# Kernel tuning notes

Measured on AMD Instinct MI355X. Metric: run time of the kernel, lower is better.

The kernel has to match this reference:

```python
import jax, jax.numpy as jnp
import numpy as np

N = 50000
E = 1600000
F_IN = 256
DIMS = 64
N_CLS = 16
R = 8


def glorot(key, shape):
    fan = shape[-2] + shape[-1] if len(shape) >= 2 else shape[-1] * 2
    std = jnp.sqrt(6.0 / fan)
    return jax.random.uniform(key, shape, jnp.float32, -std, std)


def setup_inputs() -> dict:
    key = jax.random.key(0)
    ks = jax.random.split(key, 12)
    x = jax.random.normal(ks[0], (N, F_IN), jnp.float32)
    edge_index = jax.random.randint(ks[1], (2, E), 0, N)
    edge_weight = jax.random.uniform(ks[2], (E,), jnp.float32)
    edge_color = jax.random.randint(ks[3], (E,), 0, R)
    W1 = glorot(ks[4], (R, F_IN, DIMS))
    atten1 = glorot(ks[5], (R, 2 * DIMS))
    root1 = glorot(ks[6], (F_IN, DIMS))
    bias1 = jnp.zeros((DIMS,), jnp.float32)
    W2 = glorot(ks[7], (R, DIMS, N_CLS))
    atten2 = glorot(ks[8], (R, 2 * N_CLS))
    root2 = glorot(ks[9], (DIMS, N_CLS))
    bias2 = jnp.zeros((N_CLS,), jnp.float32)
    return dict(x=x, edge_index=edge_index, edge_weight=edge_weight,
                edge_color=edge_color, W1=W1, atten1=atten1, root1=root1,
                bias1=bias1, W2=W2, atten2=atten2, root2=root2, bias2=bias2)


def wrgat_conv(x, src, dst, ew, ec, W, atten, root, bias):
    # x: [N, f_in]; W: [R, f_in, d]; atten: [R, 2d]
    d = W.shape[-1]
    xr = jnp.einsum('nf,rfd->rnd', x, W)            # [R, N, d] per-relation projection
    xi = xr[ec, dst]                                 # [E, d] dst (x_i)
    xj = xr[ec, src]                                 # [E, d] src (x_j)
    a_i = atten[:, :d][ec]                           # [E, d]
    a_j = atten[:, d:][ec]
    s = jnp.sum(a_i * xi + a_j * xj, axis=-1)        # [E]
    s = jax.nn.leaky_relu(s, 0.2)
    # segment softmax over (relation, destination) groups
    seg = ec * N + dst                               # [E], each edge belongs to one relation
    nseg = R * N
    m = jax.ops.segment_max(s, seg, num_segments=nseg)
    m = jnp.where(jnp.isfinite(m), m, 0.0)           # empty segments -> 0
    e = jnp.exp(s - m[seg])
    denom = jax.ops.segment_sum(e, seg, num_segments=nseg)
    alpha = e / jnp.maximum(denom[seg], 1e-16)
    msg = (alpha * ew)[:, None] * xj                 # [E, d]
    summed = jax.ops.segment_sum(msg, seg, num_segments=nseg).reshape(R, N, d)
    cnt = jax.ops.segment_sum(jnp.ones_like(ew), seg, num_segments=nseg).reshape(R, N, 1)
    out = (summed / jnp.maximum(cnt, 1.0)).sum(axis=0)  # mean aggr per relation, summed over relations
    return out + x @ root + bias


def reference(x, edge_index, edge_weight, edge_color, W1, atten1, root1, bias1,
              W2, atten2, root2, bias2):
    src, dst = edge_index[0], edge_index[1]          # PyG flow source_to_target: x_j=src, x_i=dst
    h = wrgat_conv(x, src, dst, edge_weight, edge_color, W1, atten1, root1, bias1)
    h = jax.nn.relu(h)                               # dropout p=0 -> identity
    h = wrgat_conv(h, src, dst, edge_weight, edge_color, W2, atten2, root2, bias2)
    return jax.nn.log_softmax(h, axis=1)
```

## Files before the change

kernel.cpp:

```cpp
#include <hip/hip_runtime.h>
#include <math.h>

#define N_NODES 50000
#define N_EDGES 1600000
#define F_IN    256
#define DIMS    64
#define N_CLS   16
#define R_REL   8
#define CAP     96

#define PROJ_BLKS 3519
#define CSR_BLKS  6250
#define FRONT_BLKS (PROJ_BLKS + CSR_BLKS)

typedef short bf16x8 __attribute__((ext_vector_type(8)));
typedef float f32x4  __attribute__((ext_vector_type(4)));

__device__ __forceinline__ unsigned short f2bf(float f) {
    unsigned u = __float_as_uint(f);
    unsigned r = (u + 0x7fffu + ((u >> 16) & 1u)) >> 16;
    return (unsigned short)r;
}
__device__ __forceinline__ float bf2f(unsigned short u) {
    return __uint_as_float(((unsigned)u) << 16);
}

__global__ __launch_bounds__(256) void cvt_x_kernel(
        const float* __restrict__ x, ushort* __restrict__ xb) {
    int i4 = blockIdx.x * 256 + threadIdx.x;
    float4 v = ((const float4*)x)[i4];
    ushort4 o;
    o.x = f2bf(v.x); o.y = f2bf(v.y); o.z = f2bf(v.z); o.w = f2bf(v.w);
    ((ushort4*)xb)[i4] = o;
}

__global__ __launch_bounds__(256) void cvt_w_kernel(
        const float* __restrict__ W1, const float* __restrict__ root1,
        ushort* __restrict__ wt1) {
    int idx = blockIdx.x * 256 + threadIdx.x;
    int r = idx >> 14, rem = idx & 16383;
    int n = rem >> 8, k = rem & 255;
    float v = (r < 8) ? W1[((size_t)r * F_IN + k) * DIMS + n]
                      : root1[(size_t)k * DIMS + n];
    wt1[idx] = f2bf(v);
}

#define BM 128
#define XPAD 72
__global__ __launch_bounds__(256, 6) void front_kernel(
        const ushort* __restrict__ xb, const ushort* __restrict__ wt1,
        const float* __restrict__ at1,
        ushort* __restrict__ xr1b, float* __restrict__ hroot,
        float* __restrict__ si1, float* __restrict__ sj1,
        const int* __restrict__ ei, const int* __restrict__ ecol,
        const float* __restrict__ ew, int* __restrict__ fill,
        int2* __restrict__ rec) {
    __shared__ ushort xs[BM][XPAD];
    const int bid = blockIdx.x;
    const int t = threadIdx.x;

    int pb = -1, cb = -1;
    if (bid < 2 * PROJ_BLKS) { if (bid & 1) cb = bid >> 1; else pb = bid >> 1; }
    else cb = PROJ_BLKS + (bid - 2 * PROJ_BLKS);

    if (cb >= 0) {
        int e = cb * 256 + t;
        int s = ei[e], d = ei[N_EDGES + e], c = ecol[e];
        float w_ = ew[e];
        int p = atomicAdd(&fill[d], 1);
        int idx = (p < CAP) ? d * CAP + p : N_NODES * CAP;
        rec[idx] = make_int2(s | (c << 16), __float_as_int(w_));
        return;
    }

    const int r = pb / 391;
    const int node0 = (pb % 391) * BM;
    const ushort* wrow = wt1 + (size_t)r * 64 * 256;

    const int w = t >> 6, lane = t & 63;
    const int lane15 = lane & 15, quad = lane >> 4;

    f32x4 acc[2][4];
    #pragma unroll
    for (int a = 0; a < 2; ++a)
        #pragma unroll
        for (int b = 0; b < 4; ++b)
            acc[a][b] = (f32x4){0.f, 0.f, 0.f, 0.f};

    for (int s = 0; s < 4; ++s) {
        __syncthreads();
        for (int i = t; i < BM * 8; i += 256) {
            int row = i >> 3, k8 = i & 7;
            int node = node0 + row;
            uint4 v = make_uint4(0, 0, 0, 0);
            if (node < N_NODES)
                v = *(const uint4*)&xb[(size_t)node * 256 + s * 64 + k8 * 8];
            *(uint4*)&xs[row][k8 * 8] = v;
        }
        __syncthreads();
        #pragma unroll
        for (int kk = 0; kk < 2; ++kk) {
            int kl = kk * 32 + quad * 8;
            bf16x8 a0 = *(const bf16x8*)&xs[w * 32 + lane15][kl];
            bf16x8 a1 = *(const bf16x8*)&xs[w * 32 + 16 + lane15][kl];
            int kg = s * 64 + kl;
            #pragma unroll
            for (int nt = 0; nt < 4; ++nt) {
                bf16x8 b = *(const bf16x8*)&wrow[(size_t)(nt * 16 + lane15) * 256 + kg];
                acc[0][nt] = __builtin_amdgcn_mfma_f32_16x16x32_bf16(a0, b, acc[0][nt], 0, 0, 0);
                acc[1][nt] = __builtin_amdgcn_mfma_f32_16x16x32_bf16(a1, b, acc[1][nt], 0, 0, 0);
            }
        }
    }

    const float* at = at1 + r * 128;
    #pragma unroll
    for (int mt = 0; mt < 2; ++mt) {
        float pi[4] = {0.f, 0.f, 0.f, 0.f};
        float pj[4] = {0.f, 0.f, 0.f, 0.f};
        #pragma unroll
        for (int nt = 0; nt < 4; ++nt) {
            int gcol = nt * 16 + lane15;
            float ai = 0.f, aj = 0.f;
            if (r < 8) { ai = at[gcol]; aj = at[64 + gcol]; }
            #pragma unroll
            for (int reg = 0; reg < 4; ++reg) {
                float v = acc[mt][nt][reg];
                int grow = node0 + w * 32 + mt * 16 + quad * 4 + reg;
                if (grow < N_NODES) {
                    if (r < 8)
                        xr1b[((size_t)r * N_NODES + grow) * 64 + gcol] = f2bf(v);
                    else
                        hroot[(size_t)grow * 64 + gcol] = v;
                }
                pi[reg] += ai * v;
                pj[reg] += aj * v;
            }
        }
        if (r < 8) {
            #pragma unroll
            for (int reg = 0; reg < 4; ++reg) {
                float s_ = pi[reg], u_ = pj[reg];
                #pragma unroll
                for (int off = 1; off < 16; off <<= 1) {
                    s_ += __shfl_xor(s_, off, 64);
                    u_ += __shfl_xor(u_, off, 64);
                }
                if (lane15 == 0) {
                    int grow = node0 + w * 32 + mt * 16 + quad * 4 + reg;
                    if (grow < N_NODES) {
                        si1[r * N_NODES + grow] = s_;
                        sj1[r * N_NODES + grow] = u_;
                    }
                }
            }
        }
    }
}

__global__ __launch_bounds__(256) void agg1s_kernel(
        const int2* __restrict__ rec, const int* __restrict__ fill,
        const float* __restrict__ si, const float* __restrict__ sj,
        const ushort* __restrict__ xr1b, const float* __restrict__ hroot,
        const float* __restrict__ bias1, float* __restrict__ h) {
    __shared__ int   esrc[4][CAP];
    __shared__ float ecoef[4][CAP];
    __shared__ float sden[4][8];
    __shared__ int   scnt[4][8];
    __shared__ float ssi[4][8];
    const int t = threadIdx.x;
    const int w = t >> 6, lane = t & 63;
    const int d = blockIdx.x * 4 + w;
    if (lane < 8) {
        sden[w][lane] = 0.f; scnt[w][lane] = 0;
        ssi[w][lane] = si[lane * N_NODES + d];
    }
    const int n = min(fill[d], CAP);
    const int base = d * CAP;
    float ex[2] = {0.f, 0.f}, ww[2] = {0.f, 0.f};
    int cc[2] = {0, 0};
    #pragma unroll
    for (int ii = 0; ii < 2; ++ii) {
        int i = lane + ii * 64;
        if (i < n) {
            int2 rc = rec[base + i];
            int s = rc.x & 0xffff, c = rc.x >> 16;
            esrc[w][i] = rc.x;
            float sc = ssi[w][c] + sj[c * N_NODES + s];
            sc = sc > 0.f ? sc : 0.2f * sc;
            float e = __expf(sc);
            ex[ii] = e; cc[ii] = c; ww[ii] = __int_as_float(rc.y);
            atomicAdd(&sden[w][c], e);
            atomicAdd(&scnt[w][c], 1);
        }
    }
    #pragma unroll
    for (int ii = 0; ii < 2; ++ii) {
        int i = lane + ii * 64;
        if (i < n)
            ecoef[w][i] = ex[ii] / fmaxf(sden[w][cc[ii]], 1e-16f)
                          * ww[ii] / (float)scnt[w][cc[ii]];
    }
    float acc0 = 0.f, acc1 = 0.f;
    int i = 0;
    for (; i + 2 <= n; i += 2) {
        int p0 = esrc[w][i], p1 = esrc[w][i + 1];
        float c0 = ecoef[w][i], c1 = ecoef[w][i + 1];
        int r0 = (p0 >> 16) * N_NODES + (p0 & 0xffff);
        int r1 = (p1 >> 16) * N_NODES + (p1 & 0xffff);
        acc0 += c0 * bf2f(xr1b[(size_t)r0 * 64 + lane]);
        acc1 += c1 * bf2f(xr1b[(size_t)r1 * 64 + lane]);
    }
    if (i < n) {
        int p0 = esrc[w][i];
        int r0 = (p0 >> 16) * N_NODES + (p0 & 0xffff);
        acc0 += ecoef[w][i] * bf2f(xr1b[(size_t)r0 * 64 + lane]);
    }
    float acc = acc0 + acc1 + hroot[(size_t)d * 64 + lane] + bias1[lane];
    h[(size_t)d * 64 + lane] = fmaxf(acc, 0.f);
}

__global__ __launch_bounds__(256) void proj2_kernel(
        const float* __restrict__ h, const float* __restrict__ W2,
        const float* __restrict__ atten2, ushort* __restrict__ xr2b,
        float* __restrict__ si2, float* __restrict__ sj2) {
    __shared__ float w2sh[8][64][16];
    __shared__ float a2sh[8][32];
    __shared__ float hsh[32][65];
    const int t = threadIdx.x;
    for (int i = t; i < R_REL * DIMS * N_CLS; i += 256)
        w2sh[i >> 10][(i >> 4) & 63][i & 15] = W2[i];
    if (t < R_REL * 2 * N_CLS) a2sh[t >> 5][t & 31] = atten2[t];
    const int node0 = blockIdx.x * 32;
    for (int i = t; i < 32 * 64; i += 256) {
        int nn = i >> 6, kk = i & 63;
        int node = node0 + nn;
        hsh[nn][kk] = (node < N_NODES) ? h[(size_t)node * 64 + kk] : 0.f;
    }
    __syncthreads();
    const int nl = t & 31, r = t >> 5;
    const int node = node0 + nl;
    float acc[16] = {};
    #pragma unroll 4
    for (int k = 0; k < 64; ++k) {
        float hv = hsh[nl][k];
        #pragma unroll
        for (int c = 0; c < 16; ++c) acc[c] += hv * w2sh[r][k][c];
    }
    if (node < N_NODES) {
        float si = 0.f, sj = 0.f;
        size_t base = ((size_t)r * N_NODES + node) * 16;
        #pragma unroll
        for (int c = 0; c < 16; ++c) {
            si += a2sh[r][c] * acc[c];
            sj += a2sh[r][16 + c] * acc[c];
        }
        #pragma unroll
        for (int c4 = 0; c4 < 4; ++c4) {
            ushort4 o;
            o.x = f2bf(acc[c4 * 4 + 0]); o.y = f2bf(acc[c4 * 4 + 1]);
            o.z = f2bf(acc[c4 * 4 + 2]); o.w = f2bf(acc[c4 * 4 + 3]);
            *(ushort4*)&xr2b[base + c4 * 4] = o;
        }
        si2[r * N_NODES + node] = si;
        sj2[r * N_NODES + node] = sj;
    }
}

__global__ __launch_bounds__(256) void agg2s_kernel(
        const int2* __restrict__ rec, const int* __restrict__ fill,
        const float* __restrict__ si, const float* __restrict__ sj,
        const ushort* __restrict__ xr2b, const float* __restrict__ h,
        const float* __restrict__ root2, const float* __restrict__ bias2,
        float* __restrict__ out) {
    __shared__ float rsh[64][17];
    __shared__ float hsh[4][64];
    __shared__ int   esrc[4][CAP];
    __shared__ float ecoef[4][CAP];
    __shared__ float sden[4][8];
    __shared__ int   scnt[4][8];
    __shared__ float ssi[4][8];
    const int t = threadIdx.x;
    for (int i = t; i < DIMS * N_CLS; i += 256) rsh[i >> 4][i & 15] = root2[i];
    const int w = t >> 6, lane = t & 63;
    const int d = blockIdx.x * 4 + w;
    hsh[w][lane] = h[(size_t)d * 64 + lane];
    if (lane < 8) {
        sden[w][lane] = 0.f; scnt[w][lane] = 0;
        ssi[w][lane] = si[lane * N_NODES + d];
    }
    const int n = min(fill[d], CAP);
    const int base = d * CAP;
    float ex[2] = {0.f, 0.f}, ww[2] = {0.f, 0.f};
    int cc[2] = {0, 0};
    #pragma unroll
    for (int ii = 0; ii < 2; ++ii) {
        int i = lane + ii * 64;
        if (i < n) {
            int2 rc = rec[base + i];
            int s = rc.x & 0xffff, c = rc.x >> 16;
            esrc[w][i] = rc.x;
            float sc = ssi[w][c] + sj[c * N_NODES + s];
            sc = sc > 0.f ? sc : 0.2f * sc;
            float e = __expf(sc);
            ex[ii] = e; cc[ii] = c; ww[ii] = __int_as_float(rc.y);
            atomicAdd(&sden[w][c], e);
            atomicAdd(&scnt[w][c], 1);
        }
    }
    #pragma unroll
    for (int ii = 0; ii < 2; ++ii) {
        int i = lane + ii * 64;
        if (i < n)
            ecoef[w][i] = ex[ii] / fmaxf(sden[w][cc[ii]], 1e-16f)
                          * ww[ii] / (float)scnt[w][cc[ii]];
    }
    __syncthreads();
    const int sub = lane >> 4, cd = lane & 15;
    float acc = 0.f;
    for (int i = sub; i < n; i += 4) {
        int p = esrc[w][i];
        int row = (p >> 16) * N_NODES + (p & 0xffff);
        acc += ecoef[w][i] * bf2f(xr2b[(size_t)row * 16 + cd]);
    }
    #pragma unroll
    for (int k0 = 0; k0 < 16; ++k0) {
        int k = sub * 16 + k0;
        acc += hsh[w][k] * rsh[k][cd];
    }
    acc += __shfl_xor(acc, 16, 64);
    acc += __shfl_xor(acc, 32, 64);
    if (sub == 0) {
        acc += bias2[cd];
        float m = acc;
        #pragma unroll
        for (int off = 8; off; off >>= 1) m = fmaxf(m, __shfl_xor(m, off, 16));
        float ex2 = expf(acc - m);
        float ssum = ex2;
        #pragma unroll
        for (int off = 8; off; off >>= 1) ssum += __shfl_xor(ssum, off, 16);
        out[(size_t)d * 16 + cd] = acc - m - logf(ssum);
    }
}

extern "C" void kernel_launch(void* const* d_in, const int* in_sizes, int n_in,
                              void* d_out, int out_size, void* d_ws, size_t ws_size,
                              hipStream_t stream) {
    const float* x     = (const float*)d_in[0];
    const int*   ei    = (const int*)  d_in[1];
    const float* ew    = (const float*)d_in[2];
    const int*   ecol  = (const int*)  d_in[3];
    const float* W1    = (const float*)d_in[4];
    const float* at1   = (const float*)d_in[5];
    const float* root1 = (const float*)d_in[6];
    const float* b1    = (const float*)d_in[7];
    const float* W2    = (const float*)d_in[8];
    const float* at2   = (const float*)d_in[9];
    const float* root2 = (const float*)d_in[10];
    const float* b2    = (const float*)d_in[11];
    float* out = (float*)d_out;
    float* ws  = (float*)d_ws;

    ushort*   xb    = (ushort*)(ws + 0);
    ushort*   wt1   = (ushort*)(ws + 6400000);
    ushort*   xr1b  = (ushort*)(ws + 6480000);
    float*    hroot = ws + 19280000;
    ushort*   xr2b  = (ushort*)(ws + 22480000);
    float*    si1   = ws + 25680000;
    float*    sj1   = ws + 26080000;
    float*    si2   = ws + 26480000;
    float*    sj2   = ws + 26880000;
    int*      fill  = (int*)(ws + 27280000);
    float*    h     = ws + 27330000;
    int2*     rec   = (int2*)(ws + 30530000);

    hipMemsetAsync(fill, 0, (size_t)N_NODES * 4, stream);

    cvt_x_kernel<<<12500, 256, 0, stream>>>(x, xb);
    cvt_w_kernel<<<576, 256, 0, stream>>>(W1, root1, wt1);
    front_kernel<<<FRONT_BLKS, 256, 0, stream>>>(xb, wt1, at1, xr1b, hroot,
                                                 si1, sj1, ei, ecol, ew, fill, rec);
    agg1s_kernel<<<12500, 256, 0, stream>>>(rec, fill, si1, sj1, xr1b, hroot, b1, h);
    proj2_kernel<<<1563, 256, 0, stream>>>(h, W2, at2, xr2b, si2, sj2);
    agg2s_kernel<<<12500, 256, 0, stream>>>(rec, fill, si2, sj2, xr2b, h, root2, b2, out);
}
```

Baseline: 447.7 us.

## Async global-to-LDS loads with XOR swizzle, nontemporal record stores, deeper gather unroll

The projection GEMM now stages x tiles through global_load_lds async copies into an XOR-swizzled, unpadded LDS layout instead of register round-trips. This removes VGPR staging and keeps LDS reads free of bank conflicts. Out-of-range rows are clamped rather than zero-filled. Edge records are packed into a 64-bit word written with a nontemporal store, and the agg1 gather loop is unrolled to four independent accumulators for more memory-level parallelism.

```diff
diff --git a/kernel.cpp b/kernel.cpp
--- a/kernel.cpp
+++ b/kernel.cpp
@@ -15,6 +15,13 @@
 
 typedef short bf16x8 __attribute__((ext_vector_type(8)));
 typedef float f32x4  __attribute__((ext_vector_type(4)));
+typedef unsigned int u32;
+typedef const __attribute__((address_space(1))) u32* gas_ptr;
+typedef __attribute__((address_space(3))) u32* las_ptr;
+
+__device__ __forceinline__ void async16(const void* g, void* l) {
+    __builtin_amdgcn_global_load_lds((gas_ptr)g, (las_ptr)l, 16, 0, 0);
+}
 
 __device__ __forceinline__ unsigned short f2bf(float f) {
     unsigned u = __float_as_uint(f);
@@ -46,7 +53,6 @@
 }
 
 #define BM 128
-#define XPAD 72
 __global__ __launch_bounds__(256, 6) void front_kernel(
         const ushort* __restrict__ xb, const ushort* __restrict__ wt1,
         const float* __restrict__ at1,
@@ -54,8 +60,8 @@
         float* __restrict__ si1, float* __restrict__ sj1,
         const int* __restrict__ ei, const int* __restrict__ ecol,
         const float* __restrict__ ew, int* __restrict__ fill,
-        int2* __restrict__ rec) {
-    __shared__ ushort xs[BM][XPAD];
+        unsigned long long* __restrict__ rec) {
+    __shared__ ushort xs[BM * 64];
     const int bid = blockIdx.x;
     const int t = threadIdx.x;
 
@@ -69,7 +75,10 @@
         float w_ = ew[e];
         int p = atomicAdd(&fill[d], 1);
         int idx = (p < CAP) ? d * CAP + p : N_NODES * CAP;
-        rec[idx] = make_int2(s | (c << 16), __float_as_int(w_));
+        unsigned long long rv =
+            ((unsigned long long)__float_as_uint(w_) << 32)
+            | (unsigned)(s | (c << 16));
+        __builtin_nontemporal_store(rv, &rec[idx]);
         return;
     }
 
@@ -79,6 +88,8 @@
 
     const int w = t >> 6, lane = t & 63;
     const int lane15 = lane & 15, quad = lane >> 4;
+    const int row0 = w * 32 + lane15;
+    const int sw0 = row0 & 7;
 
     f32x4 acc[2][4];
     #pragma unroll
@@ -89,21 +100,24 @@
 
     for (int s = 0; s < 4; ++s) {
         __syncthreads();
-        for (int i = t; i < BM * 8; i += 256) {
-            int row = i >> 3, k8 = i & 7;
+        #pragma unroll
+        for (int c = 0; c < 4; ++c) {
+            int slot = c * 256 + t;
+            int row = slot >> 3, k8p = slot & 7;
+            int k8 = k8p ^ (row & 7);
             int node = node0 + row;
-            uint4 v = make_uint4(0, 0, 0, 0);
-            if (node < N_NODES)
-                v = *(const uint4*)&xb[(size_t)node * 256 + s * 64 + k8 * 8];
-            *(uint4*)&xs[row][k8 * 8] = v;
+            if (node >= N_NODES) node = N_NODES - 1;
+            async16(&xb[(size_t)node * 256 + s * 64 + k8 * 8],
+                    &xs[(c * 256 + w * 64) * 8]);
         }
         __syncthreads();
         #pragma unroll
         for (int kk = 0; kk < 2; ++kk) {
-            int kl = kk * 32 + quad * 8;
-            bf16x8 a0 = *(const bf16x8*)&xs[w * 32 + lane15][kl];
-            bf16x8 a1 = *(const bf16x8*)&xs[w * 32 + 16 + lane15][kl];
-            int kg = s * 64 + kl;
+            int k8 = kk * 4 + quad;
+            int aidx = row0 * 64 + ((k8 ^ sw0) << 3);
+            bf16x8 a0 = *(const bf16x8*)&xs[aidx];
+            bf16x8 a1 = *(const bf16x8*)&xs[aidx + 16 * 64];
+            int kg = s * 64 + kk * 32 + quad * 8;
             #pragma unroll
             for (int nt = 0; nt < 4; ++nt) {
                 bf16x8 b = *(const bf16x8*)&wrow[(size_t)(nt * 16 + lane15) * 256 + kg];
@@ -159,7 +173,7 @@
 }
 
 __global__ __launch_bounds__(256) void agg1s_kernel(
-        const int2* __restrict__ rec, const int* __restrict__ fill,
+        const unsigned long long* __restrict__ rec, const int* __restrict__ fill,
         const float* __restrict__ si, const float* __restrict__ sj,
         const ushort* __restrict__ xr1b, const float* __restrict__ hroot,
         const float* __restrict__ bias1, float* __restrict__ h) {
@@ -183,13 +197,14 @@
     for (int ii = 0; ii < 2; ++ii) {
         int i = lane + ii * 64;
         if (i < n) {
-            int2 rc = rec[base + i];
-            int s = rc.x & 0xffff, c = rc.x >> 16;
-            esrc[w][i] = rc.x;
+            unsigned long long rv = rec[base + i];
+            int px = (int)(unsigned)rv;
+            int s = px & 0xffff, c = (px >> 16) & 0x7fff;
+            esrc[w][i] = px;
             float sc = ssi[w][c] + sj[c * N_NODES + s];
             sc = sc > 0.f ? sc : 0.2f * sc;
             float e = __expf(sc);
-            ex[ii] = e; cc[ii] = c; ww[ii] = __int_as_float(rc.y);
+            ex[ii] = e; cc[ii] = c; ww[ii] = __uint_as_float((unsigned)(rv >> 32));
             atomicAdd(&sden[w][c], e);
             atomicAdd(&scnt[w][c], 1);
         }
@@ -201,22 +216,28 @@
             ecoef[w][i] = ex[ii] / fmaxf(sden[w][cc[ii]], 1e-16f)
                           * ww[ii] / (float)scnt[w][cc[ii]];
     }
-    float acc0 = 0.f, acc1 = 0.f;
+    float a0 = 0.f, a1 = 0.f, a2 = 0.f, a3 = 0.f;
     int i = 0;
-    for (; i + 2 <= n; i += 2) {
+    for (; i + 4 <= n; i += 4) {
         int p0 = esrc[w][i], p1 = esrc[w][i + 1];
+        int p2 = esrc[w][i + 2], p3 = esrc[w][i + 3];
         float c0 = ecoef[w][i], c1 = ecoef[w][i + 1];
+        float c2 = ecoef[w][i + 2], c3 = ecoef[w][i + 3];
         int r0 = (p0 >> 16) * N_NODES + (p0 & 0xffff);
         int r1 = (p1 >> 16) * N_NODES + (p1 & 0xffff);
-        acc0 += c0 * bf2f(xr1b[(size_t)r0 * 64 + lane]);
-        acc1 += c1 * bf2f(xr1b[(size_t)r1 * 64 + lane]);
-    }
-    if (i < n) {
+        int r2 = (p2 >> 16) * N_NODES + (p2 & 0xffff);
+        int r3 = (p3 >> 16) * N_NODES + (p3 & 0xffff);
+        a0 += c0 * bf2f(xr1b[(size_t)r0 * 64 + lane]);
+        a1 += c1 * bf2f(xr1b[(size_t)r1 * 64 + lane]);
+        a2 += c2 * bf2f(xr1b[(size_t)r2 * 64 + lane]);
+        a3 += c3 * bf2f(xr1b[(size_t)r3 * 64 + lane]);
+    }
+    for (; i < n; ++i) {
         int p0 = esrc[w][i];
         int r0 = (p0 >> 16) * N_NODES + (p0 & 0xffff);
-        acc0 += ecoef[w][i] * bf2f(xr1b[(size_t)r0 * 64 + lane]);
-    }
-    float acc = acc0 + acc1 + hroot[(size_t)d * 64 + lane] + bias1[lane];
+        a0 += ecoef[w][i] * bf2f(xr1b[(size_t)r0 * 64 + lane]);
+    }
+    float acc = (a0 + a1) + (a2 + a3) + hroot[(size_t)d * 64 + lane] + bias1[lane];
     h[(size_t)d * 64 + lane] = fmaxf(acc, 0.f);
 }
 
@@ -268,7 +289,7 @@
 }
 
 __global__ __launch_bounds__(256) void agg2s_kernel(
-        const int2* __restrict__ rec, const int* __restrict__ fill,
+        const unsigned long long* __restrict__ rec, const int* __restrict__ fill,
         const float* __restrict__ si, const float* __restrict__ sj,
         const ushort* __restrict__ xr2b, const float* __restrict__ h,
         const float* __restrict__ root2, const float* __restrict__ bias2,
@@ -297,13 +318,14 @@
     for (int ii = 0; ii < 2; ++ii) {
         int i = lane + ii * 64;
         if (i < n) {
-            int2 rc = rec[base + i];
-            int s = rc.x & 0xffff, c = rc.x >> 16;
-            esrc[w][i] = rc.x;
+            unsigned long long rv = rec[base + i];
+            int px = (int)(unsigned)rv;
+            int s = px & 0xffff, c = (px >> 16) & 0x7fff;
+            esrc[w][i] = px;
             float sc = ssi[w][c] + sj[c * N_NODES + s];
             sc = sc > 0.f ? sc : 0.2f * sc;
             float e = __expf(sc);
-            ex[ii] = e; cc[ii] = c; ww[ii] = __int_as_float(rc.y);
+            ex[ii] = e; cc[ii] = c; ww[ii] = __uint_as_float((unsigned)(rv >> 32));
             atomicAdd(&sden[w][c], e);
             atomicAdd(&scnt[w][c], 1);
         }
@@ -372,7 +394,7 @@
     float*    sj2   = ws + 26880000;
     int*      fill  = (int*)(ws + 27280000);
     float*    h     = ws + 27330000;
-    int2*     rec   = (int2*)(ws + 30530000);
+    unsigned long long* rec = (unsigned long long*)(ws + 30530000);
 
     hipMemsetAsync(fill, 0, (size_t)N_NODES * 4, stream);
 
```

Measured after the change: 421.6 us. 5.8% less time.
